# Performance work log

Measured on AMD Instinct MI355X. Metric: run time of the kernel, lower is better.

The kernel has to match this reference:

```python
import jax, jax.numpy as jnp
import numpy as np

B, H, S, D = 2, 16, 2048, 64

def setup_inputs() -> dict:
    key = jax.random.key(0)
    kq, kk, kv = jax.random.split(key, 3)
    Q = jax.random.normal(kq, (B, H, S, D), dtype=jnp.float32)
    K = jax.random.normal(kk, (B, H, S, D), dtype=jnp.float32)
    V = jax.random.normal(kv, (B, H, S, D), dtype=jnp.float32)
    return {"Q": Q, "K": K, "V": V}

def reference(Q, K, V):
    # scores: [B, H, S, S]
    scale = 1.0 / jnp.sqrt(jnp.asarray(Q.shape[-1], Q.dtype))
    scores = jnp.einsum('bhqd,bhkd->bhqk', Q, K) * scale
    probs = jax.nn.softmax(scores, axis=-1)
    out = jnp.einsum('bhqk,bhkd->bhqd', probs, V)
    return out
```

## Files before the change

### kernel.cpp

```cpp
#include <hip/hip_runtime.h>
#include <hip/hip_bf16.h>


#define Bn 2
#define Hn 16
#define Sn 2048
#define Dn 64
#define OP 68

typedef __attribute__((ext_vector_type(8)))  short s16x8;
typedef __attribute__((ext_vector_type(16))) float f32x16;
typedef __attribute__((ext_vector_type(2)))  unsigned u32x2;

__device__ __forceinline__ float fast_exp2(float x) {
#if __has_builtin(__builtin_amdgcn_exp2f)
    return __builtin_amdgcn_exp2f(x);
#else
    return exp2f(x);
#endif
}
__device__ __forceinline__ unsigned short f2bf(float f) {
    unsigned u = __float_as_uint(f);
    return (unsigned short)((u + 0x7fffu + ((u >> 16) & 1u)) >> 16);
}
__device__ __forceinline__ unsigned pack2bf(float lo, float hi) {
    return (unsigned)f2bf(lo) | ((unsigned)f2bf(hi) << 16);
}
__device__ __forceinline__ unsigned cvtpk(float lo, float hi) {
    unsigned r;
    asm("v_cvt_pk_bf16_f32 %0, %1, %2" : "=v"(r) : "v"(lo), "v"(hi));
    return r;
}
__device__ __forceinline__ s16x8 reg_frag(uint4 u) {
    return __builtin_bit_cast(s16x8, u);
}

__device__ __forceinline__ void build_pf(const f32x16& c, uint4& fA, uint4& fB) {
    unsigned p01 = cvtpk(c[0], c[1]);
    unsigned p23 = cvtpk(c[2], c[3]);
    unsigned p45 = cvtpk(c[4], c[5]);
    unsigned p67 = cvtpk(c[6], c[7]);
    u32x2 s0 = __builtin_amdgcn_permlane32_swap(p01, p45, false, false);
    u32x2 s1 = __builtin_amdgcn_permlane32_swap(p23, p67, false, false);
    fA.x = s0[0]; fA.y = s1[0]; fA.z = s0[1]; fA.w = s1[1];
    unsigned p89 = cvtpk(c[8], c[9]);
    unsigned pab = cvtpk(c[10], c[11]);
    unsigned pcd = cvtpk(c[12], c[13]);
    unsigned pef = cvtpk(c[14], c[15]);
    u32x2 s2 = __builtin_amdgcn_permlane32_swap(p89, pcd, false, false);
    u32x2 s3 = __builtin_amdgcn_permlane32_swap(pab, pef, false, false);
    fB.x = s2[0]; fB.y = s3[0]; fB.z = s2[1]; fB.w = s3[1];
}

__global__ __launch_bounds__(256)
void cast_kv2(const float* __restrict__ K, const float* __restrict__ V,
              unsigned short* __restrict__ Kb, unsigned short* __restrict__ Vt) {
    __shared__ unsigned short TK[64 * 72];
    __shared__ unsigned short TV[64 * 72];
    const int tid = threadIdx.x;
    const int bh  = blockIdx.x >> 5;
    const int kt  = blockIdx.x & 31;
    const int r = tid >> 2, cc = (tid & 3) * 16;

    const size_t rowbase = ((size_t)bh * Sn + (size_t)kt * 64 + r) * Dn + cc;
    {
        const float* ks = K + rowbase;
        #pragma unroll
        for (int i = 0; i < 2; ++i) {
            float4 f0 = *(const float4*)(ks + 8 * i);
            float4 f1 = *(const float4*)(ks + 8 * i + 4);
            uint4 w;
            w.x = pack2bf(f0.x, f0.y); w.y = pack2bf(f0.z, f0.w);
            w.z = pack2bf(f1.x, f1.y); w.w = pack2bf(f1.z, f1.w);
            *(uint4*)(TK + r * 72 + cc + 8 * i) = w;
        }
    }
    {
        const float* vs = V + rowbase;
        #pragma unroll
        for (int i = 0; i < 4; ++i) {
            float4 f = *(const float4*)(vs + 4 * i);
            const int d0 = cc + 4 * i;
            TV[(d0 + 0) * 72 + r] = f2bf(f.x);
            TV[(d0 + 1) * 72 + r] = f2bf(f.y);
            TV[(d0 + 2) * 72 + r] = f2bf(f.z);
            TV[(d0 + 3) * 72 + r] = f2bf(f.w);
        }
    }
    __syncthreads();
    unsigned short* kd = Kb + ((size_t)(bh * 32 + kt) * 8) * 512;
    unsigned short* vd = Vt + ((size_t)(bh * 32 + kt) * 8) * 512;
    #pragma unroll
    for (int i = 0; i < 2; ++i) {
        const int u = i * 256 + tid;
        const int c = u >> 6, lane = u & 63;
        const int l31 = lane & 31, hf = lane >> 5;
        const int sub = c >> 2, ks = c & 3;
        const int off = (sub * 32 + l31) * 72 + ks * 16 + hf * 8;
        *(uint4*)(kd + c * 512 + lane * 8) = *(const uint4*)(TK + off);
        *(uint4*)(vd + c * 512 + lane * 8) = *(const uint4*)(TV + off);
    }
}

__global__ __launch_bounds__(128, 2)
void attn_fwd_mfma4(const float* __restrict__ Q,
                    const unsigned short* __restrict__ Kb,
                    const unsigned short* __restrict__ Vt,
                    float* __restrict__ O) {
    __shared__ __align__(16) char smem[64 * OP * 4 + 256];
    float* ob = (float*)smem;
    float* lb = ob + 64 * OP;

    const int tid  = threadIdx.x;
    const int wave = tid >> 6;
    const int lane = tid & 63;
    const int l31  = lane & 31;
    const int half = lane >> 5;

    const int bh = blockIdx.x & 31;
    const int q0 = (blockIdx.x >> 5) * 64;

    const float* Qb = Q + ((size_t)bh * Sn + q0) * Dn;
    const float FCT = 0.18033688011112042f;

    s16x8 qf[2][4];
    #pragma unroll
    for (int s = 0; s < 2; ++s) {
        const float* qp = Qb + (size_t)(s * 32 + l31) * Dn;
        #pragma unroll
        for (int ks = 0; ks < 4; ++ks) {
            const int d0 = ks * 16 + half * 8;
            float4 f0 = *(const float4*)(qp + d0);
            float4 f1 = *(const float4*)(qp + d0 + 4);
            uint4 u;
            u.x = pack2bf(f0.x * FCT, f0.y * FCT);
            u.y = pack2bf(f0.z * FCT, f0.w * FCT);
            u.z = pack2bf(f1.x * FCT, f1.y * FCT);
            u.w = pack2bf(f1.z * FCT, f1.w * FCT);
            qf[s][ks] = __builtin_bit_cast(s16x8, u);
        }
    }

    f32x16 acc00, acc01, acc10, acc11;
    #pragma unroll
    for (int r = 0; r < 16; ++r) { acc00[r]=0.f; acc01[r]=0.f; acc10[r]=0.f; acc11[r]=0.f; }
    float l0 = 0.f, l1 = 0.f;

    const unsigned short* kbase =
        Kb + ((size_t)(bh * 32 + wave * 16) * 8) * 512 + (size_t)lane * 8;
    const unsigned short* vbase =
        Vt + ((size_t)(bh * 32 + wave * 16) * 8) * 512 + (size_t)lane * 8;

    uint4 kbuf[2][8];
    #pragma unroll
    for (int c = 0; c < 8; ++c)
        kbuf[0][c] = *(const uint4*)(kbase + c * 512);

    #pragma unroll
    for (int t = 0; t < 16; ++t) {
        uint4* CUR = kbuf[t & 1];
        uint4* NXT = kbuf[(t + 1) & 1];

        uint4 vv[8];
        #pragma unroll
        for (int c = 0; c < 8; ++c)
            vv[c] = *(const uint4*)(vbase + (size_t)(t * 8 + c) * 512);
        const int tk = (t < 15 ? t + 1 : 15);
        #pragma unroll
        for (int c = 0; c < 8; ++c)
            NXT[c] = *(const uint4*)(kbase + (size_t)(tk * 8 + c) * 512);

        uint4 p00, p01, p02, p03;
        uint4 p10, p11, p12, p13;

        {
            f32x16 c0, c1;
            #pragma unroll
            for (int r = 0; r < 16; ++r) { c0[r] = 0.f; c1[r] = 0.f; }
            __builtin_amdgcn_s_setprio(1);
            #pragma unroll
            for (int ks = 0; ks < 4; ++ks) {
                c0 = __builtin_amdgcn_mfma_f32_32x32x16_bf16(reg_frag(CUR[ks]),     qf[0][ks], c0, 0, 0, 0);
                c1 = __builtin_amdgcn_mfma_f32_32x32x16_bf16(reg_frag(CUR[4 + ks]), qf[0][ks], c1, 0, 0, 0);
            }
            __builtin_amdgcn_s_setprio(0);
            #pragma unroll
            for (int r = 0; r < 16; ++r) {
                c0[r] = fast_exp2(c0[r]);
                c1[r] = fast_exp2(c1[r]);
            }
            float a0 = 0.f, a1 = 0.f, a2 = 0.f, a3 = 0.f;
            #pragma unroll
            for (int r = 0; r < 16; r += 4) {
                a0 += c0[r] + c1[r];
                a1 += c0[r + 1] + c1[r + 1];
                a2 += c0[r + 2] + c1[r + 2];
                a3 += c0[r + 3] + c1[r + 3];
            }
            l0 += (a0 + a1) + (a2 + a3);
            build_pf(c0, p00, p01);
            build_pf(c1, p02, p03);
        }

        {
            f32x16 c0, c1;
            #pragma unroll
            for (int r = 0; r < 16; ++r) { c0[r] = 0.f; c1[r] = 0.f; }
            __builtin_amdgcn_s_setprio(1);
            #pragma unroll
            for (int ks = 0; ks < 4; ++ks) {
                c0 = __builtin_amdgcn_mfma_f32_32x32x16_bf16(reg_frag(CUR[ks]),     qf[1][ks], c0, 0, 0, 0);
                c1 = __builtin_amdgcn_mfma_f32_32x32x16_bf16(reg_frag(CUR[4 + ks]), qf[1][ks], c1, 0, 0, 0);
            }
            __builtin_amdgcn_s_setprio(0);
            #pragma unroll
            for (int r = 0; r < 16; ++r) {
                c0[r] = fast_exp2(c0[r]);
                c1[r] = fast_exp2(c1[r]);
            }
            float a0 = 0.f, a1 = 0.f, a2 = 0.f, a3 = 0.f;
            #pragma unroll
            for (int r = 0; r < 16; r += 4) {
                a0 += c0[r] + c1[r];
                a1 += c0[r + 1] + c1[r + 1];
                a2 += c0[r + 2] + c1[r + 2];
                a3 += c0[r + 3] + c1[r + 3];
            }
            l1 += (a0 + a1) + (a2 + a3);
            build_pf(c0, p10, p11);
            build_pf(c1, p12, p13);
        }

        __builtin_amdgcn_s_setprio(1);
        acc00 = __builtin_amdgcn_mfma_f32_32x32x16_bf16(reg_frag(vv[0]), reg_frag(p00), acc00, 0, 0, 0);
        acc01 = __builtin_amdgcn_mfma_f32_32x32x16_bf16(reg_frag(vv[4]), reg_frag(p00), acc01, 0, 0, 0);
        acc10 = __builtin_amdgcn_mfma_f32_32x32x16_bf16(reg_frag(vv[0]), reg_frag(p10), acc10, 0, 0, 0);
        acc11 = __builtin_amdgcn_mfma_f32_32x32x16_bf16(reg_frag(vv[4]), reg_frag(p10), acc11, 0, 0, 0);
        acc00 = __builtin_amdgcn_mfma_f32_32x32x16_bf16(reg_frag(vv[1]), reg_frag(p01), acc00, 0, 0, 0);
        acc01 = __builtin_amdgcn_mfma_f32_32x32x16_bf16(reg_frag(vv[5]), reg_frag(p01), acc01, 0, 0, 0);
        acc10 = __builtin_amdgcn_mfma_f32_32x32x16_bf16(reg_frag(vv[1]), reg_frag(p11), acc10, 0, 0, 0);
        acc11 = __builtin_amdgcn_mfma_f32_32x32x16_bf16(reg_frag(vv[5]), reg_frag(p11), acc11, 0, 0, 0);
        acc00 = __builtin_amdgcn_mfma_f32_32x32x16_bf16(reg_frag(vv[2]), reg_frag(p02), acc00, 0, 0, 0);
        acc01 = __builtin_amdgcn_mfma_f32_32x32x16_bf16(reg_frag(vv[6]), reg_frag(p02), acc01, 0, 0, 0);
        acc10 = __builtin_amdgcn_mfma_f32_32x32x16_bf16(reg_frag(vv[2]), reg_frag(p12), acc10, 0, 0, 0);
        acc11 = __builtin_amdgcn_mfma_f32_32x32x16_bf16(reg_frag(vv[6]), reg_frag(p12), acc11, 0, 0, 0);
        acc00 = __builtin_amdgcn_mfma_f32_32x32x16_bf16(reg_frag(vv[3]), reg_frag(p03), acc00, 0, 0, 0);
        acc01 = __builtin_amdgcn_mfma_f32_32x32x16_bf16(reg_frag(vv[7]), reg_frag(p03), acc01, 0, 0, 0);
        acc10 = __builtin_amdgcn_mfma_f32_32x32x16_bf16(reg_frag(vv[3]), reg_frag(p13), acc10, 0, 0, 0);
        acc11 = __builtin_amdgcn_mfma_f32_32x32x16_bf16(reg_frag(vv[7]), reg_frag(p13), acc11, 0, 0, 0);
        __builtin_amdgcn_s_setprio(0);
    }

    l0 += __shfl_xor(l0, 32, 64);
    l1 += __shfl_xor(l1, 32, 64);

    __syncthreads();
    if (wave == 0) {
        #pragma unroll
        for (int g = 0; g < 4; ++g) {
            const int d0 = 8 * g + 4 * half;
            float4 f;
            f.x = acc00[4*g+0]; f.y = acc00[4*g+1]; f.z = acc00[4*g+2]; f.w = acc00[4*g+3];
            *(float4*)(ob + l31 * OP + d0) = f;
            f.x = acc01[4*g+0]; f.y = acc01[4*g+1]; f.z = acc01[4*g+2]; f.w = acc01[4*g+3];
            *(float4*)(ob + l31 * OP + d0 + 32) = f;
            f.x = acc10[4*g+0]; f.y = acc10[4*g+1]; f.z = acc10[4*g+2]; f.w = acc10[4*g+3];
            *(float4*)(ob + (32 + l31) * OP + d0) = f;
            f.x = acc11[4*g+0]; f.y = acc11[4*g+1]; f.z = acc11[4*g+2]; f.w = acc11[4*g+3];
            *(float4*)(ob + (32 + l31) * OP + d0 + 32) = f;
        }
        if (half == 0) { lb[l31] = l0; lb[32 + l31] = l1; }
    }
    __syncthreads();
    if (wave == 1) {
        const float i0 = 1.0f / (l0 + lb[l31]);
        const float i1 = 1.0f / (l1 + lb[32 + l31]);
        #pragma unroll
        for (int g = 0; g < 4; ++g) {
            const int d0 = 8 * g + 4 * half;
            float4 f;
            float* p;
            p = ob + l31 * OP + d0;            f = *(float4*)p;
            f.x = (f.x + acc00[4*g+0]) * i0; f.y = (f.y + acc00[4*g+1]) * i0;
            f.z = (f.z + acc00[4*g+2]) * i0; f.w = (f.w + acc00[4*g+3]) * i0;
            *(float4*)p = f;
            p = ob + l31 * OP + d0 + 32;       f = *(float4*)p;
            f.x = (f.x + acc01[4*g+0]) * i0; f.y = (f.y + acc01[4*g+1]) * i0;
            f.z = (f.z + acc01[4*g+2]) * i0; f.w = (f.w + acc01[4*g+3]) * i0;
            *(float4*)p = f;
            p = ob + (32 + l31) * OP + d0;     f = *(float4*)p;
            f.x = (f.x + acc10[4*g+0]) * i1; f.y = (f.y + acc10[4*g+1]) * i1;
            f.z = (f.z + acc10[4*g+2]) * i1; f.w = (f.w + acc10[4*g+3]) * i1;
            *(float4*)p = f;
            p = ob + (32 + l31) * OP + d0 + 32; f = *(float4*)p;
            f.x = (f.x + acc11[4*g+0]) * i1; f.y = (f.y + acc11[4*g+1]) * i1;
            f.z = (f.z + acc11[4*g+2]) * i1; f.w = (f.w + acc11[4*g+3]) * i1;
            *(float4*)p = f;
        }
    }
    __syncthreads();
    float* op = O + ((size_t)bh * Sn + q0) * Dn;
    #pragma unroll
    for (int it = 0; it < 8; ++it) {
        const int idx = it * 128 + tid;
        const int r = idx >> 4, c4 = (idx & 15) * 4;
        *(float4*)(op + r * Dn + c4) = *(float4*)(ob + r * OP + c4);
    }
}

extern "C" void kernel_launch(void* const* d_in, const int* in_sizes, int n_in,
                              void* d_out, int out_size, void* d_ws, size_t ws_size,
                              hipStream_t stream) {
    const float* Q = (const float*)d_in[0];
    const float* K = (const float*)d_in[1];
    const float* V = (const float*)d_in[2];
    float* O = (float*)d_out;

    const size_t elems = (size_t)Bn * Hn * Sn * Dn;
    unsigned short* Kb = (unsigned short*)d_ws;
    unsigned short* Vt = Kb + elems;

    cast_kv2<<<dim3(Bn * Hn * (Sn / 64)), dim3(256), 0, stream>>>(K, V, Kb, Vt);
    attn_fwd_mfma4<<<dim3(Bn * Hn * (Sn / 64)), dim3(128), 0, stream>>>(Q, Kb, Vt, O);
}
```

Before: 130.0 us.

## Stage K tiles through LDS via global_load_lds double buffering

```diff
diff --git a/kernel.cpp b/kernel.cpp
--- a/kernel.cpp
+++ b/kernel.cpp
@@ -33,6 +33,11 @@
 }
 __device__ __forceinline__ s16x8 reg_frag(uint4 u) {
     return __builtin_bit_cast(s16x8, u);
+}
+__device__ __forceinline__ void glds16(const unsigned short* g, char* l) {
+    __builtin_amdgcn_global_load_lds(
+        (const __attribute__((address_space(1))) void*)g,
+        (__attribute__((address_space(3))) void*)l, 16, 0, 0);
 }
 
 __device__ __forceinline__ void build_pf(const f32x16& c, uint4& fA, uint4& fB) {
@@ -107,7 +112,7 @@
                     const unsigned short* __restrict__ Kb,
                     const unsigned short* __restrict__ Vt,
                     float* __restrict__ O) {
-    __shared__ __align__(16) char smem[64 * OP * 4 + 256];
+    __shared__ __align__(16) char smem[33024];
     float* ob = (float*)smem;
     float* lb = ob + 64 * OP;
 
@@ -151,24 +156,31 @@
     const unsigned short* vbase =
         Vt + ((size_t)(bh * 32 + wave * 16) * 8) * 512 + (size_t)lane * 8;
 
-    uint4 kbuf[2][8];
+    char* myK = smem + wave * 16384;
+
     #pragma unroll
     for (int c = 0; c < 8; ++c)
-        kbuf[0][c] = *(const uint4*)(kbase + c * 512);
+        glds16(kbase + (size_t)c * 512, myK + c * 1024);
 
     #pragma unroll
     for (int t = 0; t < 16; ++t) {
-        uint4* CUR = kbuf[t & 1];
-        uint4* NXT = kbuf[(t + 1) & 1];
-
         uint4 vv[8];
         #pragma unroll
         for (int c = 0; c < 8; ++c)
             vv[c] = *(const uint4*)(vbase + (size_t)(t * 8 + c) * 512);
         const int tk = (t < 15 ? t + 1 : 15);
+        char* nbuf = myK + ((t + 1) & 1) * 8192;
         #pragma unroll
         for (int c = 0; c < 8; ++c)
-            NXT[c] = *(const uint4*)(kbase + (size_t)(tk * 8 + c) * 512);
+            glds16(kbase + (size_t)(tk * 8 + c) * 512, nbuf + c * 1024);
+        asm volatile("s_waitcnt vmcnt(16)" ::: "memory");
+        __builtin_amdgcn_sched_barrier(0);
+
+        const char* cbuf = myK + (t & 1) * 8192;
+        uint4 kk[8];
+        #pragma unroll
+        for (int c = 0; c < 8; ++c)
+            kk[c] = *(const uint4*)(cbuf + c * 1024 + (size_t)lane * 16);
 
         uint4 p00, p01, p02, p03;
         uint4 p10, p11, p12, p13;
@@ -180,8 +192,8 @@
             __builtin_amdgcn_s_setprio(1);
             #pragma unroll
             for (int ks = 0; ks < 4; ++ks) {
-                c0 = __builtin_amdgcn_mfma_f32_32x32x16_bf16(reg_frag(CUR[ks]),     qf[0][ks], c0, 0, 0, 0);
-                c1 = __builtin_amdgcn_mfma_f32_32x32x16_bf16(reg_frag(CUR[4 + ks]), qf[0][ks], c1, 0, 0, 0);
+                c0 = __builtin_amdgcn_mfma_f32_32x32x16_bf16(reg_frag(kk[ks]),     qf[0][ks], c0, 0, 0, 0);
+                c1 = __builtin_amdgcn_mfma_f32_32x32x16_bf16(reg_frag(kk[4 + ks]), qf[0][ks], c1, 0, 0, 0);
             }
             __builtin_amdgcn_s_setprio(0);
             #pragma unroll
@@ -209,8 +221,8 @@
             __builtin_amdgcn_s_setprio(1);
             #pragma unroll
             for (int ks = 0; ks < 4; ++ks) {
-                c0 = __builtin_amdgcn_mfma_f32_32x32x16_bf16(reg_frag(CUR[ks]),     qf[1][ks], c0, 0, 0, 0);
-                c1 = __builtin_amdgcn_mfma_f32_32x32x16_bf16(reg_frag(CUR[4 + ks]), qf[1][ks], c1, 0, 0, 0);
+                c0 = __builtin_amdgcn_mfma_f32_32x32x16_bf16(reg_frag(kk[ks]),     qf[1][ks], c0, 0, 0, 0);
+                c1 = __builtin_amdgcn_mfma_f32_32x32x16_bf16(reg_frag(kk[4 + ks]), qf[1][ks], c1, 0, 0, 0);
             }
             __builtin_amdgcn_s_setprio(0);
             #pragma unroll
```

Result: slower. 136.9 us (+5.3%).

## Interleave second QK^T with first PV MFMAs and vectorize V transpose staging

Applied to the files above, without the earlier changes.

```diff
diff --git a/kernel.cpp b/kernel.cpp
--- a/kernel.cpp
+++ b/kernel.cpp
@@ -78,13 +78,13 @@
     {
         const float* vs = V + rowbase;
         #pragma unroll
-        for (int i = 0; i < 4; ++i) {
-            float4 f = *(const float4*)(vs + 4 * i);
-            const int d0 = cc + 4 * i;
-            TV[(d0 + 0) * 72 + r] = f2bf(f.x);
-            TV[(d0 + 1) * 72 + r] = f2bf(f.y);
-            TV[(d0 + 2) * 72 + r] = f2bf(f.z);
-            TV[(d0 + 3) * 72 + r] = f2bf(f.w);
+        for (int i = 0; i < 2; ++i) {
+            float4 f0 = *(const float4*)(vs + 8 * i);
+            float4 f1 = *(const float4*)(vs + 8 * i + 4);
+            uint4 w;
+            w.x = pack2bf(f0.x, f0.y); w.y = pack2bf(f0.z, f0.w);
+            w.z = pack2bf(f1.x, f1.y); w.w = pack2bf(f1.z, f1.w);
+            *(uint4*)(TV + r * 72 + cc + 8 * i) = w;
         }
     }
     __syncthreads();
@@ -96,9 +96,15 @@
         const int c = u >> 6, lane = u & 63;
         const int l31 = lane & 31, hf = lane >> 5;
         const int sub = c >> 2, ks = c & 3;
-        const int off = (sub * 32 + l31) * 72 + ks * 16 + hf * 8;
-        *(uint4*)(kd + c * 512 + lane * 8) = *(const uint4*)(TK + off);
-        *(uint4*)(vd + c * 512 + lane * 8) = *(const uint4*)(TV + off);
+        const int offk = (sub * 32 + l31) * 72 + ks * 16 + hf * 8;
+        *(uint4*)(kd + c * 512 + lane * 8) = *(const uint4*)(TK + offk);
+        const int vo = (ks * 16 + hf * 8) * 72 + sub * 32 + l31;
+        uint4 wv;
+        wv.x = (unsigned)TV[vo]       | ((unsigned)TV[vo + 72]  << 16);
+        wv.y = (unsigned)TV[vo + 144] | ((unsigned)TV[vo + 216] << 16);
+        wv.z = (unsigned)TV[vo + 288] | ((unsigned)TV[vo + 360] << 16);
+        wv.w = (unsigned)TV[vo + 432] | ((unsigned)TV[vo + 504] << 16);
+        *(uint4*)(vd + c * 512 + lane * 8) = wv;
     }
 }
 
@@ -177,13 +183,11 @@
             f32x16 c0, c1;
             #pragma unroll
             for (int r = 0; r < 16; ++r) { c0[r] = 0.f; c1[r] = 0.f; }
-            __builtin_amdgcn_s_setprio(1);
             #pragma unroll
             for (int ks = 0; ks < 4; ++ks) {
                 c0 = __builtin_amdgcn_mfma_f32_32x32x16_bf16(reg_frag(CUR[ks]),     qf[0][ks], c0, 0, 0, 0);
                 c1 = __builtin_amdgcn_mfma_f32_32x32x16_bf16(reg_frag(CUR[4 + ks]), qf[0][ks], c1, 0, 0, 0);
             }
-            __builtin_amdgcn_s_setprio(0);
             #pragma unroll
             for (int r = 0; r < 16; ++r) {
                 c0[r] = fast_exp2(c0[r]);
@@ -202,53 +206,51 @@
             build_pf(c1, p02, p03);
         }
 
+        f32x16 d0, d1;
+        #pragma unroll
+        for (int r = 0; r < 16; ++r) { d0[r] = 0.f; d1[r] = 0.f; }
+        #pragma unroll
+        for (int ks = 0; ks < 4; ++ks) {
+            d0 = __builtin_amdgcn_mfma_f32_32x32x16_bf16(reg_frag(CUR[ks]),     qf[1][ks], d0, 0, 0, 0);
+            d1 = __builtin_amdgcn_mfma_f32_32x32x16_bf16(reg_frag(CUR[4 + ks]), qf[1][ks], d1, 0, 0, 0);
+        }
+
+        acc00 = __builtin_amdgcn_mfma_f32_32x32x16_bf16(reg_frag(vv[0]), reg_frag(p00), acc00, 0, 0, 0);
+        acc01 = __builtin_amdgcn_mfma_f32_32x32x16_bf16(reg_frag(vv[4]), reg_frag(p00), acc01, 0, 0, 0);
+        acc00 = __builtin_amdgcn_mfma_f32_32x32x16_bf16(reg_frag(vv[1]), reg_frag(p01), acc00, 0, 0, 0);
+        acc01 = __builtin_amdgcn_mfma_f32_32x32x16_bf16(reg_frag(vv[5]), reg_frag(p01), acc01, 0, 0, 0);
+        acc00 = __builtin_amdgcn_mfma_f32_32x32x16_bf16(reg_frag(vv[2]), reg_frag(p02), acc00, 0, 0, 0);
+        acc01 = __builtin_amdgcn_mfma_f32_32x32x16_bf16(reg_frag(vv[6]), reg_frag(p02), acc01, 0, 0, 0);
+        acc00 = __builtin_amdgcn_mfma_f32_32x32x16_bf16(reg_frag(vv[3]), reg_frag(p03), acc00, 0, 0, 0);
+        acc01 = __builtin_amdgcn_mfma_f32_32x32x16_bf16(reg_frag(vv[7]), reg_frag(p03), acc01, 0, 0, 0);
+
+        #pragma unroll
+        for (int r = 0; r < 16; ++r) {
+            d0[r] = fast_exp2(d0[r]);
+            d1[r] = fast_exp2(d1[r]);
+        }
         {
-            f32x16 c0, c1;
-            #pragma unroll
-            for (int r = 0; r < 16; ++r) { c0[r] = 0.f; c1[r] = 0.f; }
-            __builtin_amdgcn_s_setprio(1);
-            #pragma unroll
-            for (int ks = 0; ks < 4; ++ks) {
-                c0 = __builtin_amdgcn_mfma_f32_32x32x16_bf16(reg_frag(CUR[ks]),     qf[1][ks], c0, 0, 0, 0);
-                c1 = __builtin_amdgcn_mfma_f32_32x32x16_bf16(reg_frag(CUR[4 + ks]), qf[1][ks], c1, 0, 0, 0);
-            }
-            __builtin_amdgcn_s_setprio(0);
-            #pragma unroll
-            for (int r = 0; r < 16; ++r) {
-                c0[r] = fast_exp2(c0[r]);
-                c1[r] = fast_exp2(c1[r]);
-            }
             float a0 = 0.f, a1 = 0.f, a2 = 0.f, a3 = 0.f;
             #pragma unroll
             for (int r = 0; r < 16; r += 4) {
-                a0 += c0[r] + c1[r];
-                a1 += c0[r + 1] + c1[r + 1];
-                a2 += c0[r + 2] + c1[r + 2];
-                a3 += c0[r + 3] + c1[r + 3];
+                a0 += d0[r] + d1[r];
+                a1 += d0[r + 1] + d1[r + 1];
+                a2 += d0[r + 2] + d1[r + 2];
+                a3 += d0[r + 3] + d1[r + 3];
             }
             l1 += (a0 + a1) + (a2 + a3);
-            build_pf(c0, p10, p11);
-            build_pf(c1, p12, p13);
-        }
-
-        __builtin_amdgcn_s_setprio(1);
-        acc00 = __builtin_amdgcn_mfma_f32_32x32x16_bf16(reg_frag(vv[0]), reg_frag(p00), acc00, 0, 0, 0);
-        acc01 = __builtin_amdgcn_mfma_f32_32x32x16_bf16(reg_frag(vv[4]), reg_frag(p00), acc01, 0, 0, 0);
+        }
+        build_pf(d0, p10, p11);
+        build_pf(d1, p12, p13);
+
         acc10 = __builtin_amdgcn_mfma_f32_32x32x16_bf16(reg_frag(vv[0]), reg_frag(p10), acc10, 0, 0, 0);
         acc11 = __builtin_amdgcn_mfma_f32_32x32x16_bf16(reg_frag(vv[4]), reg_frag(p10), acc11, 0, 0, 0);
-        acc00 = __builtin_amdgcn_mfma_f32_32x32x16_bf16(reg_frag(vv[1]), reg_frag(p01), acc00, 0, 0, 0);
-        acc01 = __builtin_amdgcn_mfma_f32_32x32x16_bf16(reg_frag(vv[5]), reg_frag(p01), acc01, 0, 0, 0);
         acc10 = __builtin_amdgcn_mfma_f32_32x32x16_bf16(reg_frag(vv[1]), reg_frag(p11), acc10, 0, 0, 0);
         acc11 = __builtin_amdgcn_mfma_f32_32x32x16_bf16(reg_frag(vv[5]), reg_frag(p11), acc11, 0, 0, 0);
-        acc00 = __builtin_amdgcn_mfma_f32_32x32x16_bf16(reg_frag(vv[2]), reg_frag(p02), acc00, 0, 0, 0);
-        acc01 = __builtin_amdgcn_mfma_f32_32x32x16_bf16(reg_frag(vv[6]), reg_frag(p02), acc01, 0, 0, 0);
         acc10 = __builtin_amdgcn_mfma_f32_32x32x16_bf16(reg_frag(vv[2]), reg_frag(p12), acc10, 0, 0, 0);
         acc11 = __builtin_amdgcn_mfma_f32_32x32x16_bf16(reg_frag(vv[6]), reg_frag(p12), acc11, 0, 0, 0);
-        acc00 = __builtin_amdgcn_mfma_f32_32x32x16_bf16(reg_frag(vv[3]), reg_frag(p03), acc00, 0, 0, 0);
-        acc01 = __builtin_amdgcn_mfma_f32_32x32x16_bf16(reg_frag(vv[7]), reg_frag(p03), acc01, 0, 0, 0);
         acc10 = __builtin_amdgcn_mfma_f32_32x32x16_bf16(reg_frag(vv[3]), reg_frag(p13), acc10, 0, 0, 0);
         acc11 = __builtin_amdgcn_mfma_f32_32x32x16_bf16(reg_frag(vv[7]), reg_frag(p13), acc11, 0, 0, 0);
-        __builtin_amdgcn_s_setprio(0);
     }
 
     l0 += __shfl_xor(l0, 32, 64);
```

Result: slower. 137.2 us (+5.6%).
